# Optimization experiments

Measured on AMD Instinct MI355X. Metric: run time of the kernel, lower is better.

Reference implementation:

```python
import jax, jax.numpy as jnp
import numpy as np

B, CIN, H, W = 8, 64, 56, 56
COUT, K, HEADS, PAD = 64, 7, 8, 3


def hswish(x):
    return x * jnp.clip(x + 3.0, 0.0, 6.0) / 6.0


def grouped_1x1(x, w):
    # x: (B, Cin, H, W); w: (G, Cout_g, Cin_g)  -> (B, Cout, H, W)
    b, cin, h, wd = x.shape
    g = w.shape[0]
    xg = x.reshape(b, g, cin // g, h, wd)
    y = jnp.einsum('bgihw,goi->bgohw', xg, w)
    return y.reshape(b, g * w.shape[1], h, wd)


def unfold2d(x, k, h_out, w_out):
    # x: (B, C, Hp, Wp) -> (B, C, h_out, w_out, k, k), stride 1
    cols = [x[:, :, i:i + h_out, j:j + w_out] for i in range(k) for j in range(k)]
    s = jnp.stack(cols, axis=-1)  # (B,C,h,w,k*k) in (kh,kw) row-major order
    return s.reshape(*s.shape[:-1], k, k)


def setup_inputs() -> dict:
    key = jax.random.key(0)
    k1, k2, k3, k4, k5, k6 = jax.random.split(key, 6)
    cin_g, cout_g = CIN // HEADS, COUT // HEADS
    fan_out = cout_g  # 1x1 kernel, kaiming fan_out per group
    std = float(np.sqrt(2.0 / fan_out))
    return {
        'x': jax.random.normal(k1, (B, CIN, H, W), dtype=jnp.float32),
        'wq': jax.random.normal(k2, (HEADS, cout_g, cin_g), dtype=jnp.float32) * std,
        'wk': jax.random.normal(k3, (HEADS, cout_g, cin_g), dtype=jnp.float32) * std,
        'wv': jax.random.normal(k4, (HEADS, cout_g, cin_g), dtype=jnp.float32) * std,
        'rel_h': jax.random.normal(k5, (COUT // 2, 1, 1, K, 1), dtype=jnp.float32),
        'rel_w': jax.random.normal(k6, (COUT // 2, 1, 1, 1, K), dtype=jnp.float32),
    }


def reference(x, wq, wk, wv, rel_h, rel_w):
    b, _, h, w = x.shape
    heads = wq.shape[0]
    d = COUT // heads
    padded = jnp.pad(x, ((0, 0), (0, 0), (PAD, PAD), (PAD, PAD)))
    q = grouped_1x1(x, wq)                       # (B, Cout, H, W)
    k_full = grouped_1x1(padded, wk)             # (B, Cout, Hp, Wp)
    v_full = hswish(grouped_1x1(padded, wv))
    kp = unfold2d(k_full, K, h, w)               # (B, Cout, H, W, K, K)
    vp = unfold2d(v_full, K, h, w)
    kh, kw_ = kp[:, :COUT // 2], kp[:, COUT // 2:]
    kp = jnp.concatenate((kh + rel_h, kw_ + rel_w), axis=1)
    kp = kp.reshape(b, heads, d, h, w, K * K)
    vp = vp.reshape(b, heads, d, h, w, K * K)
    qh = q.reshape(b, heads, d, h, w, 1)
    # NOTE: faithful to original bug: sqrt(heads // out_channels) == 0.0
    scale = float(np.sqrt(heads // COUT))
    logits = (qh * kp).sum(axis=2, keepdims=True) * scale  # (B,heads,1,H,W,K*K)
    attn = jax.nn.softmax(logits, axis=-1)
    out = (attn * vp).sum(axis=-1)               # (B, heads, d, H, W)
    return out.reshape(b, heads * d, h, w)
```

## Files before the change

kernel.cpp:

```cpp
#include <hip/hip_runtime.h>


namespace {
constexpr int Bn = 8, CINn = 64, Hn = 56, Wn = 56;
constexpr int HEADSn = 8;
constexpr int PADn = 3;
constexpr int TH = 2;
constexpr int NTILES = Hn / TH;
constexpr int PW = Wn + 6;
constexpr int RSH = 78;
constexpr int THREADS = 128;
constexpr int NRUNS = Wn / 2;
}

__device__ __forceinline__ int sx(int x) { return x + (x >> 2); }
__device__ __forceinline__ float4 f4add(float4 a, float4 b) {
    return make_float4(a.x + b.x, a.y + b.y, a.z + b.z, a.w + b.w);
}
__device__ __forceinline__ float4 f4sub(float4 a, float4 b) {
    return make_float4(a.x - b.x, a.y - b.y, a.z - b.z, a.w - b.w);
}

__global__ __launch_bounds__(THREADS) void saconv_r4(
    const float* __restrict__ x, const float* __restrict__ wv,
    float* __restrict__ out)
{
    __shared__ float4 hs[2 * TH * RSH];

    const int bid  = blockIdx.x;
    const int tile = bid % NTILES;
    const int g    = (bid / NTILES) % HEADSn;
    const int b    = bid / (NTILES * HEADSn);
    const int h0   = tile * TH;
    const int tid  = threadIdx.x;

    const int g4 = tid >> 6;
    const int px = tid & 63;
    const int xx = px - PADn;
    const bool colok = (unsigned)xx < (unsigned)Wn;

    const float* __restrict__ wg = wv + g * 64 + g4 * 32;
    float w[32];
    #pragma unroll
    for (int i = 0; i < 32; ++i) w[i] = wg[i];

    const float* __restrict__ xg = x + (size_t)(b * CINn + g * 8) * (Hn * Wn);

    float4 s0 = make_float4(0.f, 0.f, 0.f, 0.f);
    float4 s1 = s0;
    #pragma unroll
    for (int r = 0; r < 8; ++r) {
        const int y = h0 + r - PADn;
        float4 v = make_float4(0.f, 0.f, 0.f, 0.f);
        if (colok && (unsigned)y < (unsigned)Hn) {
            float in[8];
            #pragma unroll
            for (int i = 0; i < 8; ++i)
                in[i] = xg[i * (Hn * Wn) + y * Wn + xx];
            float a[4];
            #pragma unroll
            for (int o = 0; o < 4; ++o) {
                float s = 0.f;
                #pragma unroll
                for (int i = 0; i < 8; ++i)
                    s = fmaf(w[o * 8 + i], in[i], s);
                float t = fminf(fmaxf(s + 3.f, 0.f), 6.f);
                a[o] = s * t * (1.f / 6.f);
            }
            v = make_float4(a[0], a[1], a[2], a[3]);
        }
        if (r < 7) s0 = f4add(s0, v);
        if (r >= 1) s1 = f4add(s1, v);
    }
    if (px < PW) {
        hs[(g4 * TH + 0) * RSH + sx(px)] = s0;
        hs[(g4 * TH + 1) * RSH + sx(px)] = s1;
    }
    __syncthreads();

    if (tid < TH * NRUNS * 2) {
        const int g4b = tid & 1;
        const int rem = tid >> 1;
        const int run = rem % NRUNS;
        const int y   = rem / NRUNS;
        const int x0  = run * 2;
        float4 rv[8];
        #pragma unroll
        for (int j = 0; j < 8; ++j)
            rv[j] = hs[(g4b * TH + y) * RSH + sx(x0 + j)];
        float4 t0 = rv[0];
        #pragma unroll
        for (int j = 1; j < 7; ++j) t0 = f4add(t0, rv[j]);
        float4 t1 = f4add(t0, f4sub(rv[7], rv[0]));
        const float inv = 1.f / 49.f;
        float* ob = out + ((size_t)(b * CINn + g * 8 + g4b * 4) * Hn + (h0 + y)) * Wn + x0;
        const int plane = Hn * Wn;
        float2 st;
        st.x = t0.x * inv; st.y = t1.x * inv; *(float2*)(ob + 0 * plane) = st;
        st.x = t0.y * inv; st.y = t1.y * inv; *(float2*)(ob + 1 * plane) = st;
        st.x = t0.z * inv; st.y = t1.z * inv; *(float2*)(ob + 2 * plane) = st;
        st.x = t0.w * inv; st.y = t1.w * inv; *(float2*)(ob + 3 * plane) = st;
    }
}

extern "C" void kernel_launch(void* const* d_in, const int* in_sizes, int n_in,
                              void* d_out, int out_size, void* d_ws, size_t ws_size,
                              hipStream_t stream) {
    const float* x  = (const float*)d_in[0];
    const float* wv = (const float*)d_in[3];
    float* out = (float*)d_out;

    dim3 grid(Bn * HEADSn * NTILES);
    saconv_r4<<<grid, THREADS, 0, stream>>>(x, wv, out);
}
```

Baseline: 13.30 us.

## Retile to full-height column strips with separable box sums in LDS

Each block now handles a 14-column, full-height strip for one batch and group, computing the hswish value tile once into shared memory. It then does a vertical 7-tap sliding-sum pass and a horizontal pass before writing. This removes the heavy vertical halo recompute and redundant x reads of the 2-row tiling. In exchange the grid drops to 256 blocks of 1024 threads, adds a synchronisation stage and a poorly parallel vertical pass.

```diff
diff --git a/kernel.cpp b/kernel.cpp
--- a/kernel.cpp
+++ b/kernel.cpp
@@ -5,15 +5,21 @@
 constexpr int Bn = 8, CINn = 64, Hn = 56, Wn = 56;
 constexpr int HEADSn = 8;
 constexpr int PADn = 3;
-constexpr int TH = 2;
-constexpr int NTILES = Hn / TH;
-constexpr int PW = Wn + 6;
-constexpr int RSH = 78;
-constexpr int THREADS = 128;
-constexpr int NRUNS = Wn / 2;
+constexpr int XWO = 14;
+constexpr int NSTRIP = Wn / XWO;
+constexpr int CC = XWO + 6;
+constexpr int CR = Hn + 6;
+constexpr int CSTR = 21;
+constexpr int THREADS = 1024;
+constexpr int PLANE = Hn * Wn;
 }
 
-__device__ __forceinline__ int sx(int x) { return x + (x >> 2); }
+__device__ __forceinline__ int vtIdx(int g4, int row, int col) {
+    return (g4 * CR + row) * CSTR + col;
+}
+__device__ __forceinline__ int vsIdx(int g4, int row, int col) {
+    return (g4 * Hn + row) * CSTR + col;
+}
 __device__ __forceinline__ float4 f4add(float4 a, float4 b) {
     return make_float4(a.x + b.x, a.y + b.y, a.z + b.z, a.w + b.w);
 }
@@ -21,42 +27,43 @@
     return make_float4(a.x - b.x, a.y - b.y, a.z - b.z, a.w - b.w);
 }
 
-__global__ __launch_bounds__(THREADS) void saconv_r4(
+__global__ __launch_bounds__(THREADS) void saconv_r5(
     const float* __restrict__ x, const float* __restrict__ wv,
     float* __restrict__ out)
 {
-    __shared__ float4 hs[2 * TH * RSH];
+    __shared__ float  wvs[64];
+    __shared__ float4 vt[2 * CR * CSTR];
+    __shared__ float4 vs[2 * Hn * CSTR];
 
-    const int bid  = blockIdx.x;
-    const int tile = bid % NTILES;
-    const int g    = (bid / NTILES) % HEADSn;
-    const int b    = bid / (NTILES * HEADSn);
-    const int h0   = tile * TH;
-    const int tid  = threadIdx.x;
+    const int bid   = blockIdx.x;
+    const int strip = bid & 3;
+    const int g     = (bid >> 2) & 7;
+    const int b     = bid >> 5;
+    const int x0out = strip * XWO;
+    const int tid   = threadIdx.x;
 
-    const int g4 = tid >> 6;
-    const int px = tid & 63;
-    const int xx = px - PADn;
-    const bool colok = (unsigned)xx < (unsigned)Wn;
+    if (tid < 64) wvs[tid] = wv[g * 64 + tid];
+    __syncthreads();
 
-    const float* __restrict__ wg = wv + g * 64 + g4 * 32;
+    const int g4 = tid >> 9;
+    const int t  = tid & 511;
     float w[32];
     #pragma unroll
-    for (int i = 0; i < 32; ++i) w[i] = wg[i];
+    for (int i = 0; i < 32; ++i) w[i] = wvs[g4 * 32 + i];
 
-    const float* __restrict__ xg = x + (size_t)(b * CINn + g * 8) * (Hn * Wn);
+    const float* __restrict__ xg = x + (size_t)(b * CINn + g * 8) * PLANE;
 
-    float4 s0 = make_float4(0.f, 0.f, 0.f, 0.f);
-    float4 s1 = s0;
-    #pragma unroll
-    for (int r = 0; r < 8; ++r) {
-        const int y = h0 + r - PADn;
+    for (int p = t; p < CR * CC; p += 512) {
+        const int row = p / CC;
+        const int col = p - row * CC;
+        const int y   = row - PADn;
+        const int xx  = x0out + col - PADn;
         float4 v = make_float4(0.f, 0.f, 0.f, 0.f);
-        if (colok && (unsigned)y < (unsigned)Hn) {
+        if ((unsigned)y < (unsigned)Hn && (unsigned)xx < (unsigned)Wn) {
             float in[8];
             #pragma unroll
             for (int i = 0; i < 8; ++i)
-                in[i] = xg[i * (Hn * Wn) + y * Wn + xx];
+                in[i] = xg[i * PLANE + y * Wn + xx];
             float a[4];
             #pragma unroll
             for (int o = 0; o < 4; ++o) {
@@ -64,42 +71,59 @@
                 #pragma unroll
                 for (int i = 0; i < 8; ++i)
                     s = fmaf(w[o * 8 + i], in[i], s);
-                float t = fminf(fmaxf(s + 3.f, 0.f), 6.f);
-                a[o] = s * t * (1.f / 6.f);
+                float tt = fminf(fmaxf(s + 3.f, 0.f), 6.f);
+                a[o] = s * tt * (1.f / 6.f);
             }
             v = make_float4(a[0], a[1], a[2], a[3]);
         }
-        if (r < 7) s0 = f4add(s0, v);
-        if (r >= 1) s1 = f4add(s1, v);
-    }
-    if (px < PW) {
-        hs[(g4 * TH + 0) * RSH + sx(px)] = s0;
-        hs[(g4 * TH + 1) * RSH + sx(px)] = s1;
+        vt[vtIdx(g4, row, col)] = v;
     }
     __syncthreads();
 
-    if (tid < TH * NRUNS * 2) {
-        const int g4b = tid & 1;
-        const int rem = tid >> 1;
-        const int run = rem % NRUNS;
-        const int y   = rem / NRUNS;
-        const int x0  = run * 2;
+    if (tid < 7 * 2 * CC) {
+        const int col    = tid % CC;
+        const int r      = tid / CC;
+        const int g4b    = r & 1;
+        const int rowgrp = r >> 1;
+        const int r0     = rowgrp * 8;
+        float4 win[14];
+        #pragma unroll
+        for (int j = 0; j < 14; ++j)
+            win[j] = vt[vtIdx(g4b, r0 + j, col)];
+        float4 s = win[0];
+        #pragma unroll
+        for (int j = 1; j < 7; ++j) s = f4add(s, win[j]);
+        vs[vsIdx(g4b, r0, col)] = s;
+        #pragma unroll
+        for (int k = 1; k < 8; ++k) {
+            s = f4add(s, f4sub(win[k + 6], win[k - 1]));
+            vs[vsIdx(g4b, r0 + k, col)] = s;
+        }
+    }
+    __syncthreads();
+
+    if (tid < Hn * 2 * (XWO / 2)) {
+        const int run = tid % 7;
+        const int r   = tid / 7;
+        const int g4b = r & 1;
+        const int y   = r >> 1;
+        const int xb  = run * 2;
         float4 rv[8];
         #pragma unroll
         for (int j = 0; j < 8; ++j)
-            rv[j] = hs[(g4b * TH + y) * RSH + sx(x0 + j)];
-        float4 t0 = rv[0];
+            rv[j] = vs[vsIdx(g4b, y, xb + j)];
+        float4 s0 = rv[0];
         #pragma unroll
-        for (int j = 1; j < 7; ++j) t0 = f4add(t0, rv[j]);
-        float4 t1 = f4add(t0, f4sub(rv[7], rv[0]));
+        for (int j = 1; j < 7; ++j) s0 = f4add(s0, rv[j]);
+        float4 s1 = f4add(s0, f4sub(rv[7], rv[0]));
         const float inv = 1.f / 49.f;
-        float* ob = out + ((size_t)(b * CINn + g * 8 + g4b * 4) * Hn + (h0 + y)) * Wn + x0;
-        const int plane = Hn * Wn;
+        float* ob = out + ((size_t)(b * CINn + g * 8 + g4b * 4) * Hn + y) * Wn
+                        + x0out + xb;
         float2 st;
-        st.x = t0.x * inv; st.y = t1.x * inv; *(float2*)(ob + 0 * plane) = st;
-        st.x = t0.y * inv; st.y = t1.y * inv; *(float2*)(ob + 1 * plane) = st;
-        st.x = t0.z * inv; st.y = t1.z * inv; *(float2*)(ob + 2 * plane) = st;
-        st.x = t0.w * inv; st.y = t1.w * inv; *(float2*)(ob + 3 * plane) = st;
+        st.x = s0.x * inv; st.y = s1.x * inv; *(float2*)(ob + 0 * PLANE) = st;
+        st.x = s0.y * inv; st.y = s1.y * inv; *(float2*)(ob + 1 * PLANE) = st;
+        st.x = s0.z * inv; st.y = s1.z * inv; *(float2*)(ob + 2 * PLANE) = st;
+        st.x = s0.w * inv; st.y = s1.w * inv; *(float2*)(ob + 3 * PLANE) = st;
     }
 }
 
@@ -110,6 +134,6 @@
     const float* wv = (const float*)d_in[3];
     float* out = (float*)d_out;
 
-    dim3 grid(Bn * HEADSn * NTILES);
-    saconv_r4<<<grid, THREADS, 0, stream>>>(x, wv, out);
+    dim3 grid(Bn * HEADSn * NSTRIP);
+    saconv_r5<<<grid, THREADS, 0, stream>>>(x, wv, out);
 }
```

New measurement: 12.58 us. 5.4% less time.
